# Performance work log

Hardware: AMD Instinct MI355X
Metric: run time of the kernel (lower is better)

Reference implementation:

```python
import jax, jax.numpy as jnp
import numpy as np

THRESHOLD = 1.0
DECAY = 0.9
REFRACTORY = 2.0

B, I, H, P, T, O = 4096, 512, 1024, 4, 32, 3


def setup_inputs() -> dict:
    key = jax.random.key(0)
    ks = jax.random.split(key, 14)
    s_enc = 1.0 / np.sqrt(I)
    s_lif = 1.0 / np.sqrt(I)
    s_sel = 1.0 / np.sqrt(I)
    s_o1 = 1.0 / np.sqrt(H)
    s_o2 = 1.0 / np.sqrt(H // 2)
    return {
        "x": jax.random.normal(ks[0], (B, I), jnp.float32),
        "noise": jax.random.uniform(ks[1], (B, T, I), jnp.float32),
        "num_steps": T,
        "enc_W": jax.random.uniform(ks[2], (I, I), jnp.float32, -s_enc, s_enc),
        "enc_b": jax.random.uniform(ks[3], (I,), jnp.float32, -s_enc, s_enc),
        "sel_W": jax.random.uniform(ks[4], (I, P), jnp.float32, -s_sel, s_sel),
        "sel_b": jax.random.uniform(ks[5], (P,), jnp.float32, -s_sel, s_sel),
        "lif_W": jax.random.uniform(ks[6], (P, I, H), jnp.float32, -s_lif, s_lif),
        "lif_b": jax.random.uniform(ks[7], (P, H), jnp.float32, -s_lif, s_lif),
        "out_W1": jax.random.uniform(ks[8], (H, H // 2), jnp.float32, -s_o1, s_o1),
        "out_b1": jax.random.uniform(ks[9], (H // 2,), jnp.float32, -s_o1, s_o1),
        "out_W2": jax.random.uniform(ks[10], (H // 2, O), jnp.float32, -s_o2, s_o2),
        "out_b2": jax.random.uniform(ks[11], (O,), jnp.float32, -s_o2, s_o2),
    }


def reference(x, noise, num_steps, enc_W, enc_b, sel_W, sel_b,
              lif_W, lif_b, out_W1, out_b1, out_W2, out_b2):
    dt = x.dtype
    # spike-rate encoding: Bernoulli(sigmoid(Wx+b)) sampled with external uniform noise
    encoded = jax.nn.sigmoid(x @ enc_W + enc_b)                 # [B, I]
    spike_train = (noise < encoded[:, None, :]).astype(dt)      # [B, T, I]
    spike_train = jnp.swapaxes(spike_train, 0, 1)               # [T, B, I]

    pathway_weights = jax.nn.softmax(x @ sel_W + sel_b, axis=-1)  # [B, P]

    b = x.shape[0]
    p, h = lif_b.shape
    mem0 = jnp.zeros((p, b, h), dt)
    ref0 = jnp.zeros((p, b, h), dt)
    acc0 = jnp.zeros((b, h), dt)

    def step(carry, sp):
        mem, ref, acc = carry
        current = jnp.einsum('bi,pih->pbh', sp, lif_W) + lif_b[:, None, :]
        mem = DECAY * mem + current
        not_ref = (ref == 0).astype(dt)
        spikes = (mem >= THRESHOLD).astype(dt) * not_ref        # [P, B, H]
        mem = mem * (1.0 - spikes)
        ref = jnp.maximum(ref - 1.0 + spikes * REFRACTORY, 0.0)
        acc = acc + jnp.einsum('pbh,bp->bh', spikes, pathway_weights)
        return (mem, ref, acc), None

    (_, _, acc), _ = jax.lax.scan(step, (mem0, ref0, acc0), spike_train)
    mean_spike_rate = acc / jnp.asarray(num_steps, dt)          # [B, H]

    hid = jax.nn.relu(mean_spike_rate @ out_W1 + out_b1)
    output = hid @ out_W2 + out_b2                              # [B, O]
    return output, pathway_weights, mean_spike_rate
```

## Files before the change

kernel.cpp:

```cpp
#include <hip/hip_runtime.h>
#include <hip/hip_bf16.h>
#include <stdint.h>
#include <cstdio>
#include <math.h>


typedef unsigned int u32;
typedef unsigned long long u64;

#define ENCT_OFF 0u
#define BITS_OFF (8u << 20)
#define WT_OFF   (16u << 20)
#define CB_OFF   (24u << 20)
#define HID_OFF  (88u << 20)
#define WS_NEED  ((size_t)HID_OFF + (8u << 20))

#define OUT1_F 12288
#define OUT2_F 28672

__global__ __launch_bounds__(64) void k_genc(const float* __restrict__ x,
                                             const float* __restrict__ W,
                                             const float* __restrict__ bias,
                                             float* __restrict__ encT) {
  const int lane = threadIdx.x;
  const int bg = blockIdx.x & 63;
  const int jg = blockIdx.x >> 6;
  const int b = bg * 64 + lane;
  const int j0 = jg * 8;
  const float* xr = x + (size_t)b * 512;
  float accA[8], accB[8];
#pragma unroll
  for (int u = 0; u < 8; ++u) { accA[u] = 0.0f; accB[u] = 0.0f; }
  for (int k = 0; k < 384; ++k) {
    float xv = xr[k];
#pragma unroll
    for (int u = 0; u < 8; ++u) accA[u] = fmaf(xv, W[k * 512 + j0 + u], accA[u]);
  }
  for (int k = 384; k < 512; ++k) {
    float xv = xr[k];
#pragma unroll
    for (int u = 0; u < 8; ++u) accB[u] = fmaf(xv, W[k * 512 + j0 + u], accB[u]);
  }
#pragma unroll
  for (int u = 0; u < 8; ++u) {
    float z = __fadd_rn(__fadd_rn(accA[u], accB[u]), bias[j0 + u]);
    float ef = (float)exp(-(double)z);
    float enc = 1.0f / (1.0f + ef);
    encT[(size_t)(j0 + u) * 4096 + b] = enc;
  }
}

__global__ __launch_bounds__(64) void k_spike(const float* __restrict__ noise,
                                              const float* __restrict__ encT,
                                              u64* __restrict__ bitsP) {
  const int lane = threadIdx.x;
  const int t = blockIdx.x & 31;
  const int bw = blockIdx.x >> 5;
  const int b = bw * 64 + lane;
  const float* nr = noise + ((size_t)b * 32 + t) * 512;
  u64* dst = bitsP + (((size_t)bw * 4 + (t >> 3)) * 512) * 8 + (t & 7);
  for (int i0 = 0; i0 < 512; i0 += 4) {
    float4 nv = *(const float4*)(nr + i0);
    float e0 = encT[(size_t)(i0 + 0) * 4096 + b];
    float e1 = encT[(size_t)(i0 + 1) * 4096 + b];
    float e2 = encT[(size_t)(i0 + 2) * 4096 + b];
    float e3 = encT[(size_t)(i0 + 3) * 4096 + b];
    u64 m0 = __ballot(nv.x < e0);
    u64 m1 = __ballot(nv.y < e1);
    u64 m2 = __ballot(nv.z < e2);
    u64 m3 = __ballot(nv.w < e3);
    if (lane == 0) {
      dst[(i0 + 0) * 8] = m0; dst[(i0 + 1) * 8] = m1;
      dst[(i0 + 2) * 8] = m2; dst[(i0 + 3) * 8] = m3;
    }
  }
}

__global__ __launch_bounds__(256) void k_wrep(const float* __restrict__ lifW,
                                              float* __restrict__ Wt) {
  int idx = blockIdx.x * 256 + threadIdx.x;
  int i = idx & 511;
  int hs = (idx >> 9) & 127;
  int p = idx >> 16;
  const float* src = lifW + ((size_t)(p * 512 + i)) * 1024 + hs * 8;
  float4 a = *(const float4*)src;
  float4 c = *(const float4*)(src + 4);
  float* dst = Wt + (((size_t)(p * 128 + hs)) * 512 + (size_t)i) * 8;
  *(float4*)dst = a;
  *(float4*)(dst + 4) = c;
}

__global__ __launch_bounds__(256) void k_sel(const float* __restrict__ x,
                                             const float* __restrict__ selW,
                                             const float* __restrict__ selB,
                                             float* __restrict__ out1) {
  int b = blockIdx.x * 256 + threadIdx.x;
  const float* xr = x + (size_t)b * 512;
  double a0 = 0, a1 = 0, a2 = 0, a3 = 0;
  for (int k = 0; k < 512; ++k) {
    double xv = (double)xr[k];
    float4 w = *(const float4*)(selW + k * 4);
    a0 = fma(xv, (double)w.x, a0);
    a1 = fma(xv, (double)w.y, a1);
    a2 = fma(xv, (double)w.z, a2);
    a3 = fma(xv, (double)w.w, a3);
  }
  a0 += (double)selB[0]; a1 += (double)selB[1];
  a2 += (double)selB[2]; a3 += (double)selB[3];
  double m = fmax(fmax(a0, a1), fmax(a2, a3));
  double e0 = exp(a0 - m), e1 = exp(a1 - m), e2 = exp(a2 - m), e3 = exp(a3 - m);
  double inv = 1.0 / (e0 + e1 + e2 + e3);
  float4 wf = {(float)(e0 * inv), (float)(e1 * inv), (float)(e2 * inv), (float)(e3 * inv)};
  *(float4*)(out1 + (size_t)b * 4) = wf;
}

__global__ __launch_bounds__(64, 4) void k_lif(const float* __restrict__ Wt,
                                               const float* __restrict__ lifB,
                                               const u64* __restrict__ bitsP,
                                               u32* __restrict__ cb) {
  const int lane = threadIdx.x;
  const int bid = blockIdx.x;
  const int xcd = bid & 7;
  const int idx = bid >> 3;
  const int slab = xcd * 64 + (idx & 63);
  const int bw = idx >> 6;
  const int p = slab >> 7;
  const int h0 = (slab & 127) * 8;
  const int b0 = bw * 64;
  const float* wbase = Wt + (size_t)slab * 512 * 8;
  const u64* mbase = bitsP + ((size_t)bw * 4) * 512 * 8;
  const float* biasp = lifB + p * 1024 + h0;

  float mem[8], bias_r[8];
  u32 cbits[8];
#pragma unroll
  for (int h = 0; h < 8; ++h) {
    mem[h] = 0.0f; cbits[h] = 0u;
    bias_r[h] = biasp[h];
  }

#pragma unroll 1
  for (int tg = 0; tg < 4; ++tg) {
    float acc[8][8];
#pragma unroll
    for (int tt = 0; tt < 8; ++tt)
#pragma unroll
      for (int h = 0; h < 8; ++h) acc[tt][h] = 0.0f;

    const u64* mrow = mbase + (size_t)tg * 512 * 8;
#pragma unroll 2
    for (int i = 0; i < 512; ++i) {
      const float* wr = wbase + (size_t)i * 8;
      const u64* mr = mrow + (size_t)i * 8;
      float spf[8];
#pragma unroll
      for (int tt = 0; tt < 8; ++tt)
        asm("v_cndmask_b32 %0, 0, 1.0, %1" : "=v"(spf[tt]) : "s"(mr[tt]));
#pragma unroll
      for (int tt = 0; tt < 8; ++tt)
#pragma unroll
        for (int h = 0; h < 8; ++h)
          acc[tt][h] = fmaf(wr[h], spf[tt], acc[tt][h]);
    }
#pragma unroll
    for (int tt = 0; tt < 8; ++tt) {
      const int t = tg * 8 + tt;
#pragma unroll
      for (int h = 0; h < 8; ++h) {
        float c = __fadd_rn(acc[tt][h], bias_r[h]);
        float mo = mem[h];
        bool blocked = (__float_as_uint(mo) == 0x80000000u);
        float mn = __fadd_rn(__fmul_rn(mo, 0.9f), c);
        bool sp = (mn >= 1.0f) && (!blocked);
        mem[h] = sp ? -0.0f : mn;
        cbits[h] |= (sp ? 1u : 0u) << t;
      }
    }
  }
  u32* dst = cb + ((size_t)p * 4096 + b0 + lane) * 1024 + h0;
  uint4 v0 = {cbits[0], cbits[1], cbits[2], cbits[3]};
  uint4 v1 = {cbits[4], cbits[5], cbits[6], cbits[7]};
  *(uint4*)dst = v0;
  *(uint4*)(dst + 4) = v1;
}

__global__ __launch_bounds__(256) void k_reduce(const u32* __restrict__ cb,
                                                const float* __restrict__ w,
                                                float* __restrict__ msr) {
  int idx = blockIdx.x * 256 + threadIdx.x;
  int h = idx & 1023;
  int b = idx >> 10;
  float4 wv = *(const float4*)(w + (size_t)b * 4);
  u32 c0 = cb[((size_t)0 * 4096 + b) * 1024 + h];
  u32 c1 = cb[((size_t)1 * 4096 + b) * 1024 + h];
  u32 c2 = cb[((size_t)2 * 4096 + b) * 1024 + h];
  u32 c3 = cb[((size_t)3 * 4096 + b) * 1024 + h];
  float acc = 0.0f;
#pragma unroll
  for (int t = 0; t < 32; ++t) {
    float s = ((c0 >> t) & 1u) ? wv.x : 0.0f;
    s = __fadd_rn(s, ((c1 >> t) & 1u) ? wv.y : 0.0f);
    s = __fadd_rn(s, ((c2 >> t) & 1u) ? wv.z : 0.0f);
    s = __fadd_rn(s, ((c3 >> t) & 1u) ? wv.w : 0.0f);
    acc = __fadd_rn(acc, s);
  }
  msr[(size_t)b * 1024 + h] = acc * 0.03125f;
}

__global__ __launch_bounds__(256) void k_gemm_relu(const float* __restrict__ A, int lda,
                                                   const float* __restrict__ W, int ldw,
                                                   const float* __restrict__ bias,
                                                   float* __restrict__ out, int ldo, int K) {
  __shared__ float As[16][65];
  __shared__ float Bs[16][64];
  const int tid = threadIdx.x;
  const int tx = tid & 15, ty = tid >> 4;
  const int n0 = blockIdx.x * 64, m0 = blockIdx.y * 64;
  const int sm = tid >> 2, skq = tid & 3;
  float acc[4][4] = {};
  for (int k0 = 0; k0 < K; k0 += 16) {
    float4 av = *(const float4*)(A + (size_t)(m0 + sm) * lda + k0 + skq * 4);
    As[skq * 4 + 0][sm] = av.x;
    As[skq * 4 + 1][sm] = av.y;
    As[skq * 4 + 2][sm] = av.z;
    As[skq * 4 + 3][sm] = av.w;
#pragma unroll
    for (int j = 0; j < 4; ++j) {
      int k = j * 4 + (tid >> 6);
      int n = tid & 63;
      Bs[k][n] = W[(size_t)(k0 + k) * ldw + n0 + n];
    }
    __syncthreads();
#pragma unroll
    for (int k = 0; k < 16; ++k) {
      float a[4], bb[4];
#pragma unroll
      for (int i = 0; i < 4; ++i) a[i] = As[k][ty * 4 + i];
#pragma unroll
      for (int i = 0; i < 4; ++i) bb[i] = Bs[k][tx * 4 + i];
#pragma unroll
      for (int i = 0; i < 4; ++i)
#pragma unroll
        for (int ii = 0; ii < 4; ++ii) acc[i][ii] = fmaf(a[i], bb[ii], acc[i][ii]);
    }
    __syncthreads();
  }
#pragma unroll
  for (int i = 0; i < 4; ++i)
#pragma unroll
    for (int ii = 0; ii < 4; ++ii) {
      float v = fmaxf(acc[i][ii] + bias[n0 + tx * 4 + ii], 0.0f);
      out[(size_t)(m0 + ty * 4 + i) * ldo + n0 + tx * 4 + ii] = v;
    }
}

__global__ __launch_bounds__(256) void k_head2(const float* __restrict__ hid,
                                               const float* __restrict__ W2,
                                               const float* __restrict__ b2,
                                               float* __restrict__ out0) {
  __shared__ float w2s[512][3];
  int tid = threadIdx.x;
  for (int i = tid; i < 1536; i += 256) ((float*)w2s)[i] = W2[i];
  __syncthreads();
  int b = blockIdx.x * 256 + tid;
  const float* hr = hid + (size_t)b * 512;
  float a0 = 0, a1 = 0, a2 = 0;
  for (int j = 0; j < 512; ++j) {
    float h = hr[j];
    a0 = fmaf(h, w2s[j][0], a0);
    a1 = fmaf(h, w2s[j][1], a1);
    a2 = fmaf(h, w2s[j][2], a2);
  }
  out0[b * 3 + 0] = a0 + b2[0];
  out0[b * 3 + 1] = a1 + b2[1];
  out0[b * 3 + 2] = a2 + b2[2];
}

extern "C" void kernel_launch(void* const* d_in, const int* in_sizes, int n_in,
                              void* d_out, int out_size, void* d_ws, size_t ws_size,
                              hipStream_t stream) {
  const float* x = (const float*)d_in[0];
  const float* noise = (const float*)d_in[1];
  const float* encW = (const float*)d_in[3];
  const float* encB = (const float*)d_in[4];
  const float* selW = (const float*)d_in[5];
  const float* selB = (const float*)d_in[6];
  const float* lifW = (const float*)d_in[7];
  const float* lifB = (const float*)d_in[8];
  const float* W1 = (const float*)d_in[9];
  const float* b1 = (const float*)d_in[10];
  const float* W2 = (const float*)d_in[11];
  const float* b2 = (const float*)d_in[12];
  float* out = (float*)d_out;
  unsigned char* ws = (unsigned char*)d_ws;

  if (ws_size < WS_NEED) {
    fprintf(stderr, "kernel_launch: ws too small (%zu < %zu)\n", ws_size, (size_t)WS_NEED);
    return;
  }

  float* encT = (float*)(ws + ENCT_OFF);
  u64* bitsP = (u64*)(ws + BITS_OFF);
  float* Wt = (float*)(ws + WT_OFF);
  u32* cb = (u32*)(ws + CB_OFF);
  float* hid = (float*)(ws + HID_OFF);

  k_genc<<<dim3(4096), 64, 0, stream>>>(x, encW, encB, encT);
  k_sel<<<dim3(16), 256, 0, stream>>>(x, selW, selB, out + OUT1_F);
  k_wrep<<<dim3(1024), 256, 0, stream>>>(lifW, Wt);
  k_spike<<<dim3(2048), 64, 0, stream>>>(noise, encT, bitsP);
  k_lif<<<dim3(32768), 64, 0, stream>>>(Wt, lifB, bitsP, cb);
  k_reduce<<<dim3(16384), 256, 0, stream>>>(cb, out + OUT1_F, out + OUT2_F);
  k_gemm_relu<<<dim3(8, 64), 256, 0, stream>>>(out + OUT2_F, 1024, W1, 512, b1, hid, 512, 1024);
  k_head2<<<dim3(16), 256, 0, stream>>>(hid, W2, b2, out);
}
```

Measured before the change: 7.937 ms.

## Pre-expand spike bitmasks into per-lane byte vectors for LIF kernel

Adds a k_expand kernel that turns the wave-level 64-bit ballot masks into a per-(i,batch) 8-byte vector holding one spike byte per time step. k_lif then loads one u64 per lane per input and converts the bytes to floats, instead of doing eight scalar mask loads and cndmasks. The block-to-slab mapping is also simplified from the XCD-aware swizzle to a plain linear one. In exchange it writes and reads a 64 MB intermediate buffer and adds per-lane global loads, and dropping the XCD swizzle may reduce L2 reuse of the weight slabs.

```diff
diff --git a/kernel.cpp b/kernel.cpp
--- a/kernel.cpp
+++ b/kernel.cpp
@@ -11,8 +11,9 @@
 #define ENCT_OFF 0u
 #define BITS_OFF (8u << 20)
 #define WT_OFF   (16u << 20)
-#define CB_OFF   (24u << 20)
-#define HID_OFF  (88u << 20)
+#define SPF_OFF  (24u << 20)
+#define CB_OFF   (88u << 20)
+#define HID_OFF  (152u << 20)
 #define WS_NEED  ((size_t)HID_OFF + (8u << 20))
 
 #define OUT1_F 12288
@@ -76,6 +77,26 @@
   }
 }
 
+__global__ __launch_bounds__(64) void k_expand(const u64* __restrict__ bitsP,
+                                               unsigned char* __restrict__ spf) {
+  const int lane = threadIdx.x;
+  const int bid = blockIdx.x;
+  const int ic = bid & 7;
+  const int tg = (bid >> 3) & 3;
+  const int bw = bid >> 5;
+  const u64* src = bitsP + (((size_t)bw * 4 + tg) * 512) * 8;
+  for (int ii = 0; ii < 64; ++ii) {
+    const int i = ic * 64 + ii;
+    u64 w = 0;
+#pragma unroll
+    for (int tt = 0; tt < 8; ++tt) {
+      u64 m = src[(size_t)i * 8 + tt];
+      w |= ((m >> lane) & 1ULL) << (8 * tt);
+    }
+    *(u64*)(spf + ((size_t)(tg * 512 + i) * 4096 + bw * 64 + lane) * 8) = w;
+  }
+}
+
 __global__ __launch_bounds__(256) void k_wrep(const float* __restrict__ lifW,
                                               float* __restrict__ Wt) {
   int idx = blockIdx.x * 256 + threadIdx.x;
@@ -116,19 +137,16 @@
 
 __global__ __launch_bounds__(64, 4) void k_lif(const float* __restrict__ Wt,
                                                const float* __restrict__ lifB,
-                                               const u64* __restrict__ bitsP,
+                                               const unsigned char* __restrict__ spf,
                                                u32* __restrict__ cb) {
   const int lane = threadIdx.x;
   const int bid = blockIdx.x;
-  const int xcd = bid & 7;
-  const int idx = bid >> 3;
-  const int slab = xcd * 64 + (idx & 63);
-  const int bw = idx >> 6;
+  const int slab = bid & 511;
+  const int bw = bid >> 9;
   const int p = slab >> 7;
   const int h0 = (slab & 127) * 8;
   const int b0 = bw * 64;
   const float* wbase = Wt + (size_t)slab * 512 * 8;
-  const u64* mbase = bitsP + ((size_t)bw * 4) * 512 * 8;
   const float* biasp = lifB + p * 1024 + h0;
 
   float mem[8], bias_r[8];
@@ -147,20 +165,35 @@
 #pragma unroll
       for (int h = 0; h < 8; ++h) acc[tt][h] = 0.0f;
 
-    const u64* mrow = mbase + (size_t)tg * 512 * 8;
+    const unsigned char* sb = spf + ((size_t)(tg * 512) * 4096 + b0 + lane) * 8;
+
 #pragma unroll 2
     for (int i = 0; i < 512; ++i) {
-      const float* wr = wbase + (size_t)i * 8;
-      const u64* mr = mrow + (size_t)i * 8;
-      float spf[8];
-#pragma unroll
-      for (int tt = 0; tt < 8; ++tt)
-        asm("v_cndmask_b32 %0, 0, 1.0, %1" : "=v"(spf[tt]) : "s"(mr[tt]));
-#pragma unroll
-      for (int tt = 0; tt < 8; ++tt)
-#pragma unroll
-        for (int h = 0; h < 8; ++h)
-          acc[tt][h] = fmaf(wr[h], spf[tt], acc[tt][h]);
+      u64 sv = *(const u64*)(sb + (size_t)i * 32768);
+      float4 w0 = *(const float4*)(wbase + i * 8);
+      float4 w1 = *(const float4*)(wbase + i * 8 + 4);
+      u32 lo = (u32)sv, hi = (u32)(sv >> 32);
+      float s0 = (float)(lo & 0xffu);
+      float s1 = (float)((lo >> 8) & 0xffu);
+      float s2 = (float)((lo >> 16) & 0xffu);
+      float s3 = (float)(lo >> 24);
+      float s4 = (float)(hi & 0xffu);
+      float s5 = (float)((hi >> 8) & 0xffu);
+      float s6 = (float)((hi >> 16) & 0xffu);
+      float s7 = (float)(hi >> 24);
+      float sarr[8] = {s0, s1, s2, s3, s4, s5, s6, s7};
+#pragma unroll
+      for (int tt = 0; tt < 8; ++tt) {
+        float sp = sarr[tt];
+        acc[tt][0] = fmaf(w0.x, sp, acc[tt][0]);
+        acc[tt][1] = fmaf(w0.y, sp, acc[tt][1]);
+        acc[tt][2] = fmaf(w0.z, sp, acc[tt][2]);
+        acc[tt][3] = fmaf(w0.w, sp, acc[tt][3]);
+        acc[tt][4] = fmaf(w1.x, sp, acc[tt][4]);
+        acc[tt][5] = fmaf(w1.y, sp, acc[tt][5]);
+        acc[tt][6] = fmaf(w1.z, sp, acc[tt][6]);
+        acc[tt][7] = fmaf(w1.w, sp, acc[tt][7]);
+      }
     }
 #pragma unroll
     for (int tt = 0; tt < 8; ++tt) {
@@ -302,6 +335,7 @@
   float* encT = (float*)(ws + ENCT_OFF);
   u64* bitsP = (u64*)(ws + BITS_OFF);
   float* Wt = (float*)(ws + WT_OFF);
+  unsigned char* spf = ws + SPF_OFF;
   u32* cb = (u32*)(ws + CB_OFF);
   float* hid = (float*)(ws + HID_OFF);
 
@@ -309,7 +343,8 @@
   k_sel<<<dim3(16), 256, 0, stream>>>(x, selW, selB, out + OUT1_F);
   k_wrep<<<dim3(1024), 256, 0, stream>>>(lifW, Wt);
   k_spike<<<dim3(2048), 64, 0, stream>>>(noise, encT, bitsP);
-  k_lif<<<dim3(32768), 64, 0, stream>>>(Wt, lifB, bitsP, cb);
+  k_expand<<<dim3(2048), 64, 0, stream>>>(bitsP, spf);
+  k_lif<<<dim3(32768), 64, 0, stream>>>(Wt, lifB, spf, cb);
   k_reduce<<<dim3(16384), 256, 0, stream>>>(cb, out + OUT1_F, out + OUT2_F);
   k_gemm_relu<<<dim3(8, 64), 256, 0, stream>>>(out + OUT2_F, 1024, W1, 512, b1, hid, 512, 1024);
   k_head2<<<dim3(16), 256, 0, stream>>>(hid, W2, b2, out);
```

Measured after the change: 6.421 ms. 1.24x faster.
